# Kernel optimization log

Hardware: AMD Instinct MI355X
Metric: run time of the kernel (lower is better)

Reference implementation:

```python
import jax, jax.numpy as jnp
import numpy as np

D = 1024
H = 16
DK = D // H
MLP = 4096
EPS = 1e-5


def layernorm(x, w, b):
    mu = jnp.mean(x, axis=-1, keepdims=True)
    var = jnp.mean(jnp.square(x - mu), axis=-1, keepdims=True)
    return (x - mu) * jax.lax.rsqrt(var + EPS) * w + b


def setup_inputs() -> dict:
    key = jax.random.key(0)
    ks = jax.random.split(key, 12)
    s = 0.02
    return {
        "x": jax.random.normal(ks[0], (8, 1024, D), dtype=jnp.float32),
        "ln1_w": jnp.ones((D,), jnp.float32),
        "ln1_b": jnp.zeros((D,), jnp.float32),
        "wq": jax.random.normal(ks[1], (D, D), jnp.float32) * s,
        "bq": jnp.zeros((D,), jnp.float32),
        "wk": jax.random.normal(ks[2], (D, D), jnp.float32) * s,
        "bk": jnp.zeros((D,), jnp.float32),
        "wv": jax.random.normal(ks[3], (D, D), jnp.float32) * s,
        "bv": jnp.zeros((D,), jnp.float32),
        "wo": jax.random.normal(ks[4], (D, D), jnp.float32) * s,
        "bo": jnp.zeros((D,), jnp.float32),
        "ln2_w": jnp.ones((D,), jnp.float32),
        "ln2_b": jnp.zeros((D,), jnp.float32),
        "w1": jax.random.normal(ks[5], (D, MLP), jnp.float32) * s,
        "b1": jnp.zeros((MLP,), jnp.float32),
        "w2": jax.random.normal(ks[6], (MLP, D), jnp.float32) * s,
        "b2": jnp.zeros((D,), jnp.float32),
    }


def reference(x, ln1_w, ln1_b, wq, bq, wk, bk, wv, bv, wo, bo, ln2_w, ln2_b, w1, b1, w2, b2):
    B, S, _ = x.shape
    h = layernorm(x, ln1_w, ln1_b)
    # QKV projections, split heads: [B, H, S, DK]
    q = (h @ wq + bq).reshape(B, S, H, DK).transpose(0, 2, 1, 3)
    k = (h @ wk + bk).reshape(B, S, H, DK).transpose(0, 2, 1, 3)
    v = (h @ wv + bv).reshape(B, S, H, DK).transpose(0, 2, 1, 3)
    scores = jnp.einsum('bhqd,bhkd->bhqk', q, k) / np.sqrt(DK).astype(np.float32)
    attn = jax.nn.softmax(scores, axis=-1)
    ctx = jnp.einsum('bhqk,bhkd->bhqd', attn, v)
    ctx = ctx.transpose(0, 2, 1, 3).reshape(B, S, D)
    # NOTE: original MultiHeadAttention applies ReLU after the output projection
    attn_out = jax.nn.relu(ctx @ wo + bo)
    out1 = x + attn_out  # dropout is identity in eval
    h2 = layernorm(out1, ln2_w, ln2_b)
    ff = jax.nn.gelu(h2 @ w1 + b1, approximate=False) @ w2 + b2
    return out1 + ff
```

## Files before the change

### kernel.cpp

```cpp
#include <hip/hip_runtime.h>
#include <hip/hip_bf16.h>
#include <math.h>

typedef __bf16 bf16x8 __attribute__((ext_vector_type(8)));
typedef __bf16 bf16x4 __attribute__((ext_vector_type(4)));
typedef float f32x4 __attribute__((ext_vector_type(4)));

typedef __attribute__((address_space(3))) unsigned int lds_u32_t;
typedef __attribute__((address_space(1))) const unsigned int glb_u32_t;

static __device__ __forceinline__ f32x4 mfma16(bf16x8 a, bf16x8 b, f32x4 c) {
  return __builtin_amdgcn_mfma_f32_16x16x32_bf16(a, b, c, 0, 0, 0);
}

static __device__ __forceinline__ float fast_exp2(float x) {
#if __has_builtin(__builtin_amdgcn_exp2f)
  return __builtin_amdgcn_exp2f(x);
#else
  return exp2f(x);
#endif
}

static __device__ __forceinline__ void load_lds16(const __bf16* g, __bf16* l) {
  __builtin_amdgcn_global_load_lds((glb_u32_t*)g, (lds_u32_t*)l, 16, 0, 0);
}

__global__ __launch_bounds__(256) void transpose_w(const float* __restrict__ src,
                                                   __bf16* __restrict__ dst,
                                                   int R, int C) {
  __shared__ float tile[32][33];
  int tx = threadIdx.x, ty = threadIdx.y;
  int c0 = blockIdx.x * 32, r0 = blockIdx.y * 32;
#pragma unroll
  for (int i = 0; i < 4; i++)
    tile[ty + 8 * i][tx] = src[(size_t)(r0 + ty + 8 * i) * C + c0 + tx];
  __syncthreads();
#pragma unroll
  for (int i = 0; i < 4; i++)
    dst[(size_t)(c0 + ty + 8 * i) * R + r0 + tx] = (__bf16)tile[tx][ty + 8 * i];
}

__global__ __launch_bounds__(256) void ln_kernel(const float* __restrict__ x,
                                                 const float* __restrict__ w,
                                                 const float* __restrict__ b,
                                                 __bf16* __restrict__ out) {
  int row = blockIdx.x, tid = threadIdx.x;
  const float* xr = x + (size_t)row * 1024;
  float v[4];
  float s = 0.f, sq = 0.f;
#pragma unroll
  for (int i = 0; i < 4; i++) {
    v[i] = xr[tid + 256 * i];
    s += v[i];
    sq += v[i] * v[i];
  }
#pragma unroll
  for (int off = 1; off < 64; off <<= 1) {
    s += __shfl_xor(s, off, 64);
    sq += __shfl_xor(sq, off, 64);
  }
  __shared__ float red[8];
  int wave = tid >> 6, lane = tid & 63;
  if (lane == 0) { red[wave] = s; red[4 + wave] = sq; }
  __syncthreads();
  if (tid == 0) {
    float S = red[0] + red[1] + red[2] + red[3];
    float SQ = red[4] + red[5] + red[6] + red[7];
    float mu = S * (1.f / 1024.f);
    float var = SQ * (1.f / 1024.f) - mu * mu;
    red[0] = mu;
    red[1] = rsqrtf(var + 1e-5f);
  }
  __syncthreads();
  float mu = red[0], rstd = red[1];
  __bf16* orow = out + (size_t)row * 1024;
#pragma unroll
  for (int i = 0; i < 4; i++) {
    int c = tid + 256 * i;
    orow[c] = (__bf16)((v[i] - mu) * rstd * w[c] + b[c]);
  }
}

enum { MODE_QKV = 0, MODE_WO = 3, MODE_F1 = 4, MODE_F2 = 5 };

template <int MODE>
__global__ __launch_bounds__(256, 2) void gemm_bt(const __bf16* __restrict__ A,
                                                  const __bf16* __restrict__ Bt,
                                                  const float* __restrict__ b0,
                                                  const float* __restrict__ b1,
                                                  const float* __restrict__ b2,
                                                  const float* __restrict__ aux,
                                                  void* __restrict__ o0,
                                                  void* __restrict__ o1,
                                                  void* __restrict__ o2,
                                                  int N, int K) {
  __shared__ __align__(16) __bf16 As[128 * 64];
  __shared__ __align__(16) __bf16 Bs[128 * 64];
  const int tid = threadIdx.x;
  const int m0 = blockIdx.y * 128, n0 = blockIdx.x * 128;
  const int wave = tid >> 6, lane = tid & 63, quad = lane >> 4, l16 = lane & 15;
  const int wm = (wave >> 1) * 64, wn = (wave & 1) * 64;

  int srow[4], sgran[4];
#pragma unroll
  for (int i = 0; i < 4; i++) {
    int inst = wave * 4 + i;
    srow[i] = inst * 8 + (lane >> 3);
    sgran[i] = (lane & 7) ^ (srow[i] & 7);
  }

  const f32x4 zero4 = {0.f, 0.f, 0.f, 0.f};
  f32x4 acc[4][4];
#pragma unroll
  for (int i = 0; i < 4; i++)
#pragma unroll
    for (int j = 0; j < 4; j++) acc[i][j] = zero4;

  for (int kt = 0; kt < K; kt += 64) {
#pragma unroll
    for (int i = 0; i < 4; i++) {
      int inst = wave * 4 + i;
      load_lds16(&A[(size_t)(m0 + srow[i]) * K + kt + sgran[i] * 8], &As[inst * 512]);
      load_lds16(&Bt[(size_t)(n0 + srow[i]) * K + kt + sgran[i] * 8], &Bs[inst * 512]);
    }
    __syncthreads();
#pragma unroll
    for (int ks = 0; ks < 64; ks += 32) {
      bf16x8 af[4], bfv[4];
#pragma unroll
      for (int mi = 0; mi < 4; mi++) {
        int row = wm + 16 * mi + l16;
        int pg = ((ks >> 3) + quad) ^ (row & 7);
        af[mi] = *(const bf16x8*)&As[row * 64 + pg * 8];
      }
#pragma unroll
      for (int ni = 0; ni < 4; ni++) {
        int row = wn + 16 * ni + l16;
        int pg = ((ks >> 3) + quad) ^ (row & 7);
        bfv[ni] = *(const bf16x8*)&Bs[row * 64 + pg * 8];
      }
#pragma unroll
      for (int mi = 0; mi < 4; mi++)
#pragma unroll
        for (int ni = 0; ni < 4; ni++)
          acc[mi][ni] = mfma16(af[mi], bfv[ni], acc[mi][ni]);
    }
    __syncthreads();
  }

  int seg = (n0 >> 10);
  const float* bsel = (MODE == MODE_QKV) ? (seg == 0 ? b0 : seg == 1 ? b1 : b2) : b0;

#pragma unroll
  for (int mi = 0; mi < 4; mi++) {
#pragma unroll
    for (int ni = 0; ni < 4; ni++) {
      int ncol = n0 + wn + 16 * ni + l16;
      int cc = ncol & 1023;
      float bval = bsel[(MODE == MODE_QKV) ? cc : ncol];
#pragma unroll
      for (int r = 0; r < 4; r++) {
        int m = m0 + wm + 16 * mi + quad * 4 + r;
        float val = acc[mi][ni][r] + bval;
        if constexpr (MODE == MODE_QKV) {
          int bb = m >> 10, s = m & 1023, h = cc >> 6, dk = cc & 63;
          if (seg == 0)
            ((__bf16*)o0)[(((size_t)(bb * 16 + h)) * 1024 + s) * 64 + dk] =
                (__bf16)(val * 0.18033688011112042f);
          else if (seg == 1)
            ((__bf16*)o1)[(((size_t)(bb * 16 + h)) * 1024 + s) * 64 + dk] = (__bf16)val;
          else
            ((__bf16*)o2)[(((size_t)(bb * 16 + h)) * 64 + dk) * 1024 + s] = (__bf16)val;
        } else if constexpr (MODE == MODE_WO) {
          val = fmaxf(val, 0.f);
          size_t idx = (size_t)m * 1024 + ncol;
          ((float*)o0)[idx] = aux[idx] + val;
        } else if constexpr (MODE == MODE_F1) {
          float g = 0.5f * val * (1.f + erff(val * 0.70710678118654752f));
          ((__bf16*)o0)[(size_t)m * 4096 + ncol] = (__bf16)g;
        } else {
          size_t idx = (size_t)m * 1024 + ncol;
          ((float*)o0)[idx] = aux[idx] + val;
        }
      }
    }
  }
}

template <int MODE>
__global__ __launch_bounds__(512, 2) void gemm256(const __bf16* __restrict__ A,
                                                  const __bf16* __restrict__ Bt,
                                                  const float* __restrict__ b0,
                                                  const float* __restrict__ b1,
                                                  const float* __restrict__ b2,
                                                  const float* __restrict__ aux,
                                                  void* __restrict__ o0,
                                                  void* __restrict__ o1,
                                                  void* __restrict__ o2,
                                                  int N, int K) {
  __shared__ __align__(16) __bf16 As[4][8192];
  __shared__ __align__(16) __bf16 Bs[4][8192];
  const int tid = threadIdx.x;
  const int m0 = blockIdx.y * 256, n0 = blockIdx.x * 256;
  const int wave = tid >> 6, lane = tid & 63, quad = lane >> 4, l16 = lane & 15;
  const int wr = wave >> 2, wc = wave & 3;

  const int Lsub = lane >> 3;
  const int sp = (lane & 7) ^ Lsub;
  const int par = sp & 1, kq = sp >> 1;
  const int rbase = wave * 16 + 2 * Lsub + par;
  const __bf16* pA0 = A + (size_t)(m0 + rbase) * K + 8 * kq;
  const __bf16* pA1 = A + (size_t)(m0 + rbase + 128) * K + 8 * kq;
  const __bf16* pB0 = Bt + (size_t)(n0 + rbase) * K + 8 * kq;
  const __bf16* pB1 = Bt + (size_t)(n0 + rbase + 128) * K + 8 * kq;
  const int dst0 = (wave * 8) * 64;
  const int dst1 = (64 + wave * 8) * 64;

  int afOff[8], bfOff[4];
#pragma unroll
  for (int mi = 0; mi < 8; mi++) {
    int r = wr * 128 + 16 * mi + l16;
    int L = r >> 1;
    int sl = (2 * quad + (r & 1)) ^ (L & 7);
    afOff[mi] = L * 128 + sl * 16;
  }
#pragma unroll
  for (int nj = 0; nj < 4; nj++) {
    int c = wc * 64 + 16 * nj + l16;
    int L = c >> 1;
    int sl = (2 * quad + (c & 1)) ^ (L & 7);
    bfOff[nj] = L * 128 + sl * 16;
  }

  const f32x4 zero4 = {0.f, 0.f, 0.f, 0.f};
  f32x4 acc[8][4];
#pragma unroll
  for (int i = 0; i < 8; i++)
#pragma unroll
    for (int j = 0; j < 4; j++) acc[i][j] = zero4;

  const int nt = K >> 5;

  auto stage = [&](int t) {
    int slot = t & 3;
    __bf16* a = &As[slot][0];
    __bf16* b = &Bs[slot][0];
    load_lds16(pA0, a + dst0);
    load_lds16(pA1, a + dst1);
    load_lds16(pB0, b + dst0);
    load_lds16(pB1, b + dst1);
    pA0 += 32; pA1 += 32; pB0 += 32; pB1 += 32;
  };

  auto window = [&](int t, bool dostage) {
    const char* ab = (const char*)&As[t & 3][0];
    const char* bb = (const char*)&Bs[t & 3][0];
    bf16x8 af[8], bfv[4];
#pragma unroll
    for (int mi = 0; mi < 8; mi++) af[mi] = *(const bf16x8*)(ab + afOff[mi]);
#pragma unroll
    for (int nj = 0; nj < 4; nj++) bfv[nj] = *(const bf16x8*)(bb + bfOff[nj]);
    if (dostage) stage(t + 3);
    __builtin_amdgcn_s_setprio(1);
#pragma unroll
    for (int mi = 0; mi < 8; mi++)
#pragma unroll
      for (int nj = 0; nj < 4; nj++)
        acc[mi][nj] = mfma16(af[mi], bfv[nj], acc[mi][nj]);
    __builtin_amdgcn_s_setprio(0);
  };

  stage(0);
  stage(1);
  stage(2);
  asm volatile("s_waitcnt vmcnt(8)" ::: "memory");
  __builtin_amdgcn_s_barrier();
  __builtin_amdgcn_sched_barrier(0);

  for (int t = 0; t < nt - 3; ++t) {
    window(t, true);
    asm volatile("s_waitcnt vmcnt(8)" ::: "memory");
    __builtin_amdgcn_s_barrier();
    __builtin_amdgcn_sched_barrier(0);
  }
  window(nt - 3, false);
  asm volatile("s_waitcnt vmcnt(4)" ::: "memory");
  __builtin_amdgcn_s_barrier();
  __builtin_amdgcn_sched_barrier(0);
  window(nt - 2, false);
  asm volatile("s_waitcnt vmcnt(0)" ::: "memory");
  __builtin_amdgcn_s_barrier();
  __builtin_amdgcn_sched_barrier(0);
  window(nt - 1, false);

  int seg = (n0 >> 10);
  const float* bsel = (MODE == MODE_QKV) ? (seg == 0 ? b0 : seg == 1 ? b1 : b2) : b0;

#pragma unroll
  for (int mi = 0; mi < 8; mi++) {
#pragma unroll
    for (int nj = 0; nj < 4; nj++) {
      int ncol = n0 + wc * 64 + 16 * nj + l16;
      int cc = ncol & 1023;
      float bval = bsel[(MODE == MODE_QKV) ? cc : ncol];
#pragma unroll
      for (int r = 0; r < 4; r++) {
        int m = m0 + wr * 128 + 16 * mi + quad * 4 + r;
        float val = acc[mi][nj][r] + bval;
        if constexpr (MODE == MODE_QKV) {
          int bb = m >> 10, s = m & 1023, h = cc >> 6, dk = cc & 63;
          if (seg == 0)
            ((__bf16*)o0)[(((size_t)(bb * 16 + h)) * 1024 + s) * 64 + dk] =
                (__bf16)(val * 0.18033688011112042f);
          else if (seg == 1)
            ((__bf16*)o1)[(((size_t)(bb * 16 + h)) * 1024 + s) * 64 + dk] = (__bf16)val;
          else
            ((__bf16*)o2)[(((size_t)(bb * 16 + h)) * 64 + dk) * 1024 + s] = (__bf16)val;
        } else if constexpr (MODE == MODE_WO) {
          val = fmaxf(val, 0.f);
          size_t idx = (size_t)m * 1024 + ncol;
          ((float*)o0)[idx] = aux[idx] + val;
        } else if constexpr (MODE == MODE_F1) {
          float g = 0.5f * val * (1.f + erff(val * 0.70710678118654752f));
          ((__bf16*)o0)[(size_t)m * 4096 + ncol] = (__bf16)g;
        } else {
          size_t idx = (size_t)m * 1024 + ncol;
          ((float*)o0)[idx] = aux[idx] + val;
        }
      }
    }
  }
}

__global__ __launch_bounds__(256) void attn_kernel(const __bf16* __restrict__ Q,
                                                   const __bf16* __restrict__ Kp,
                                                   const __bf16* __restrict__ Vt,
                                                   __bf16* __restrict__ ctx) {
  __shared__ __align__(16) __bf16 Ps[2][4][32][72];
  const int tid = threadIdx.x;
  const int bh = blockIdx.x, qb = blockIdx.y;
  const int wave = tid >> 6, lane = tid & 63, quad = lane >> 4, l16 = lane & 15;
  const int qrow0 = qb * 128 + wave * 32;

  bf16x8 aq[2][2];
#pragma unroll
  for (int mi = 0; mi < 2; mi++) {
    const __bf16* qrow = Q + ((size_t)bh * 1024 + qrow0 + mi * 16 + l16) * 64;
    aq[mi][0] = *(const bf16x8*)&qrow[8 * quad];
    aq[mi][1] = *(const bf16x8*)&qrow[32 + 8 * quad];
  }

  const f32x4 zero4 = {0.f, 0.f, 0.f, 0.f};
  f32x4 o[2][4];
  float lp[2] = {0.f, 0.f};
#pragma unroll
  for (int mi = 0; mi < 2; mi++)
#pragma unroll
    for (int nj = 0; nj < 4; nj++) o[mi][nj] = zero4;

  const __bf16* kb0 = Kp + (size_t)bh * 65536;
  const __bf16* vb0 = Vt + (size_t)bh * 65536;

  bf16x8 kfA[4][2], kfB[4][2];
#pragma unroll
  for (int ni = 0; ni < 4; ni++) {
    const __bf16* krow = kb0 + (16 * ni + l16) * 64;
    kfA[ni][0] = *(const bf16x8*)&krow[8 * quad];
    kfA[ni][1] = *(const bf16x8*)&krow[32 + 8 * quad];
  }

  auto body = [&](int kbk, int buf, bf16x8 (&kcur)[4][2], bf16x8 (&knxt)[4][2]) {
    bf16x8 vf[2][4];
#pragma unroll
    for (int half = 0; half < 2; half++)
#pragma unroll
      for (int nj = 0; nj < 4; nj++)
        vf[half][nj] = *(const bf16x8*)(vb0 + (size_t)(nj * 16 + l16) * 1024 +
                                        kbk * 64 + 32 * half + 8 * quad);
    if (kbk < 15) {
      const __bf16* kbase = kb0 + (kbk + 1) * 4096;
#pragma unroll
      for (int ni = 0; ni < 4; ni++) {
        const __bf16* krow = kbase + (16 * ni + l16) * 64;
        knxt[ni][0] = *(const bf16x8*)&krow[8 * quad];
        knxt[ni][1] = *(const bf16x8*)&krow[32 + 8 * quad];
      }
    }
    f32x4 st[2][4];
    __builtin_amdgcn_s_setprio(1);
#pragma unroll
    for (int mi = 0; mi < 2; mi++)
#pragma unroll
      for (int ni = 0; ni < 4; ni++) {
        st[mi][ni] = mfma16(kcur[ni][0], aq[mi][0], zero4);
        st[mi][ni] = mfma16(kcur[ni][1], aq[mi][1], st[mi][ni]);
      }
    __builtin_amdgcn_s_setprio(0);
#pragma unroll
    for (int mi = 0; mi < 2; mi++)
#pragma unroll
      for (int ni = 0; ni < 4; ni++) {
        union { bf16x4 v4; __bf16 b[4]; } pk;
#pragma unroll
        for (int r = 0; r < 4; r++) {
          float p = fast_exp2(st[mi][ni][r]);
          lp[mi] += p;
          pk.b[r] = (__bf16)p;
        }
        *(bf16x4*)&Ps[buf][wave][16 * mi + l16][16 * ni + 4 * quad] = pk.v4;
      }
    bf16x8 pa[2][2];
#pragma unroll
    for (int mi = 0; mi < 2; mi++) {
      pa[mi][0] = *(const bf16x8*)&Ps[buf][wave][16 * mi + l16][8 * quad];
      pa[mi][1] = *(const bf16x8*)&Ps[buf][wave][16 * mi + l16][32 + 8 * quad];
    }
    __builtin_amdgcn_s_setprio(1);
#pragma unroll
    for (int mi = 0; mi < 2; mi++)
#pragma unroll
      for (int nj = 0; nj < 4; nj++) {
        o[mi][nj] = mfma16(pa[mi][0], vf[0][nj], o[mi][nj]);
        o[mi][nj] = mfma16(pa[mi][1], vf[1][nj], o[mi][nj]);
      }
    __builtin_amdgcn_s_setprio(0);
  };

  for (int kbk2 = 0; kbk2 < 16; kbk2 += 2) {
    body(kbk2, 0, kfA, kfB);
    body(kbk2 + 1, 1, kfB, kfA);
  }

#pragma unroll
  for (int mi = 0; mi < 2; mi++) {
    lp[mi] += __shfl_xor(lp[mi], 16, 64);
    lp[mi] += __shfl_xor(lp[mi], 32, 64);
  }

  int bb = bh >> 4, h = bh & 15;
#pragma unroll
  for (int mi = 0; mi < 2; mi++)
#pragma unroll
    for (int r = 0; r < 4; r++) {
      float inv = 1.f / __shfl(lp[mi], 4 * quad + r, 64);
      int s = qrow0 + mi * 16 + 4 * quad + r;
#pragma unroll
      for (int nj = 0; nj < 4; nj++)
        ctx[((size_t)(bb * 1024 + s)) * 1024 + h * 64 + nj * 16 + l16] =
            (__bf16)(o[mi][nj][r] * inv);
    }
}

extern "C" void kernel_launch(void* const* d_in, const int* in_sizes, int n_in,
                              void* d_out, int out_size, void* d_ws, size_t ws_size,
                              hipStream_t stream) {
  const float* x = (const float*)d_in[0];
  const float* ln1w = (const float*)d_in[1];
  const float* ln1b = (const float*)d_in[2];
  const float* wq = (const float*)d_in[3];
  const float* bq = (const float*)d_in[4];
  const float* wk = (const float*)d_in[5];
  const float* bk = (const float*)d_in[6];
  const float* wv = (const float*)d_in[7];
  const float* bv = (const float*)d_in[8];
  const float* wo = (const float*)d_in[9];
  const float* bo = (const float*)d_in[10];
  const float* ln2w = (const float*)d_in[11];
  const float* ln2b = (const float*)d_in[12];
  const float* w1 = (const float*)d_in[13];
  const float* b1 = (const float*)d_in[14];
  const float* w2 = (const float*)d_in[15];
  const float* b2 = (const float*)d_in[16];
  float* out = (float*)d_out;

  char* ws = (char*)d_ws;
  const size_t MB = 1024 * 1024;
  __bf16* wqkv_t = (__bf16*)(ws + 0 * MB);
  __bf16* wq_t = (__bf16*)(ws + 0 * MB);
  __bf16* wk_t = (__bf16*)(ws + 2 * MB);
  __bf16* wv_t = (__bf16*)(ws + 4 * MB);
  __bf16* wo_t = (__bf16*)(ws + 6 * MB);
  __bf16* w1_t = (__bf16*)(ws + 8 * MB);
  __bf16* w2_t = (__bf16*)(ws + 16 * MB);
  __bf16* hbuf = (__bf16*)(ws + 24 * MB);
  __bf16* qbuf = (__bf16*)(ws + 40 * MB);
  __bf16* kbuf = (__bf16*)(ws + 56 * MB);
  __bf16* vtbuf = (__bf16*)(ws + 72 * MB);
  __bf16* ctxbuf = (__bf16*)(ws + 88 * MB);
  __bf16* ff1 = (__bf16*)(ws + 40 * MB);

  dim3 tb(32, 8);
  transpose_w<<<dim3(32, 32), tb, 0, stream>>>(wq, wq_t, 1024, 1024);
  transpose_w<<<dim3(32, 32), tb, 0, stream>>>(wk, wk_t, 1024, 1024);
  transpose_w<<<dim3(32, 32), tb, 0, stream>>>(wv, wv_t, 1024, 1024);
  transpose_w<<<dim3(32, 32), tb, 0, stream>>>(wo, wo_t, 1024, 1024);
  transpose_w<<<dim3(128, 32), tb, 0, stream>>>(w1, w1_t, 1024, 4096);
  transpose_w<<<dim3(32, 128), tb, 0, stream>>>(w2, w2_t, 4096, 1024);

  ln_kernel<<<8192, 256, 0, stream>>>(x, ln1w, ln1b, hbuf);

  gemm256<MODE_QKV><<<dim3(12, 32), 512, 0, stream>>>(
      hbuf, wqkv_t, bq, bk, bv, nullptr, qbuf, kbuf, vtbuf, 3072, 1024);

  attn_kernel<<<dim3(128, 8), 256, 0, stream>>>(qbuf, kbuf, vtbuf, ctxbuf);

  gemm_bt<MODE_WO><<<dim3(8, 64), 256, 0, stream>>>(
      ctxbuf, wo_t, bo, nullptr, nullptr, x, out, nullptr, nullptr, 1024, 1024);

  ln_kernel<<<8192, 256, 0, stream>>>(out, ln2w, ln2b, hbuf);

  gemm256<MODE_F1><<<dim3(16, 32), 512, 0, stream>>>(
      hbuf, w1_t, b1, nullptr, nullptr, nullptr, ff1, nullptr, nullptr, 4096, 1024);
  gemm_bt<MODE_F2><<<dim3(8, 64), 256, 0, stream>>>(
      ff1, w2_t, b2, nullptr, nullptr, out, out, nullptr, nullptr, 1024, 4096);
}
```

Baseline: 595.2 us.

## Halve attention query tile per wave and double grid for occupancy

The attention kernel now handles 16 query rows per wave instead of 32, doubles the grid along the query axis, and adds a launch-bounds occupancy hint of 4 blocks. K and V fragments are prefetched one key block ahead inside a simple loop rather than a ping-pong lambda. The aim is to cut register pressure and raise occupancy to hide global-load latency. The cost is that each K/V fragment is reused by half as many query rows, so K/V global traffic doubles.

```diff
diff --git a/kernel.cpp b/kernel.cpp
--- a/kernel.cpp
+++ b/kernel.cpp
@@ -332,123 +332,108 @@
   }
 }
 
-__global__ __launch_bounds__(256) void attn_kernel(const __bf16* __restrict__ Q,
-                                                   const __bf16* __restrict__ Kp,
-                                                   const __bf16* __restrict__ Vt,
-                                                   __bf16* __restrict__ ctx) {
-  __shared__ __align__(16) __bf16 Ps[2][4][32][72];
+__global__ __launch_bounds__(256, 4) void attn_kernel(const __bf16* __restrict__ Q,
+                                                      const __bf16* __restrict__ Kp,
+                                                      const __bf16* __restrict__ Vt,
+                                                      __bf16* __restrict__ ctx) {
+  __shared__ __align__(16) __bf16 Ps[2][4][16][72];
   const int tid = threadIdx.x;
   const int bh = blockIdx.x, qb = blockIdx.y;
   const int wave = tid >> 6, lane = tid & 63, quad = lane >> 4, l16 = lane & 15;
-  const int qrow0 = qb * 128 + wave * 32;
-
-  bf16x8 aq[2][2];
-#pragma unroll
-  for (int mi = 0; mi < 2; mi++) {
-    const __bf16* qrow = Q + ((size_t)bh * 1024 + qrow0 + mi * 16 + l16) * 64;
-    aq[mi][0] = *(const bf16x8*)&qrow[8 * quad];
-    aq[mi][1] = *(const bf16x8*)&qrow[32 + 8 * quad];
+  const int qrow0 = qb * 64 + wave * 16;
+
+  bf16x8 aq[2];
+  {
+    const __bf16* qrow = Q + ((size_t)bh * 1024 + qrow0 + l16) * 64;
+    aq[0] = *(const bf16x8*)&qrow[8 * quad];
+    aq[1] = *(const bf16x8*)&qrow[32 + 8 * quad];
   }
 
   const f32x4 zero4 = {0.f, 0.f, 0.f, 0.f};
-  f32x4 o[2][4];
-  float lp[2] = {0.f, 0.f};
-#pragma unroll
-  for (int mi = 0; mi < 2; mi++)
-#pragma unroll
-    for (int nj = 0; nj < 4; nj++) o[mi][nj] = zero4;
+  f32x4 o[4];
+  float lp = 0.f;
+#pragma unroll
+  for (int nj = 0; nj < 4; nj++) o[nj] = zero4;
 
   const __bf16* kb0 = Kp + (size_t)bh * 65536;
   const __bf16* vb0 = Vt + (size_t)bh * 65536;
 
-  bf16x8 kfA[4][2], kfB[4][2];
+  bf16x8 kf[4][2], vf[2][4];
 #pragma unroll
   for (int ni = 0; ni < 4; ni++) {
     const __bf16* krow = kb0 + (16 * ni + l16) * 64;
-    kfA[ni][0] = *(const bf16x8*)&krow[8 * quad];
-    kfA[ni][1] = *(const bf16x8*)&krow[32 + 8 * quad];
-  }
-
-  auto body = [&](int kbk, int buf, bf16x8 (&kcur)[4][2], bf16x8 (&knxt)[4][2]) {
-    bf16x8 vf[2][4];
-#pragma unroll
-    for (int half = 0; half < 2; half++)
-#pragma unroll
-      for (int nj = 0; nj < 4; nj++)
-        vf[half][nj] = *(const bf16x8*)(vb0 + (size_t)(nj * 16 + l16) * 1024 +
-                                        kbk * 64 + 32 * half + 8 * quad);
-    if (kbk < 15) {
-      const __bf16* kbase = kb0 + (kbk + 1) * 4096;
+    kf[ni][0] = *(const bf16x8*)&krow[8 * quad];
+    kf[ni][1] = *(const bf16x8*)&krow[32 + 8 * quad];
+  }
+#pragma unroll
+  for (int half = 0; half < 2; half++)
+#pragma unroll
+    for (int nj = 0; nj < 4; nj++)
+      vf[half][nj] = *(const bf16x8*)(vb0 + (size_t)(nj * 16 + l16) * 1024 +
+                                      32 * half + 8 * quad);
+
+  for (int t = 0; t < 16; ++t) {
+    const int buf = t & 1;
+    f32x4 st[4];
+    __builtin_amdgcn_s_setprio(1);
+#pragma unroll
+    for (int ni = 0; ni < 4; ni++) {
+      st[ni] = mfma16(kf[ni][0], aq[0], zero4);
+      st[ni] = mfma16(kf[ni][1], aq[1], st[ni]);
+    }
+    __builtin_amdgcn_s_setprio(0);
+    if (t < 15) {
+      const __bf16* kbase = kb0 + (t + 1) * 4096;
 #pragma unroll
       for (int ni = 0; ni < 4; ni++) {
         const __bf16* krow = kbase + (16 * ni + l16) * 64;
-        knxt[ni][0] = *(const bf16x8*)&krow[8 * quad];
-        knxt[ni][1] = *(const bf16x8*)&krow[32 + 8 * quad];
+        kf[ni][0] = *(const bf16x8*)&krow[8 * quad];
+        kf[ni][1] = *(const bf16x8*)&krow[32 + 8 * quad];
       }
     }
-    f32x4 st[2][4];
+#pragma unroll
+    for (int ni = 0; ni < 4; ni++) {
+      union { bf16x4 v4; __bf16 b[4]; } pk;
+#pragma unroll
+      for (int r = 0; r < 4; r++) {
+        float p = fast_exp2(st[ni][r]);
+        lp += p;
+        pk.b[r] = (__bf16)p;
+      }
+      *(bf16x4*)&Ps[buf][wave][l16][16 * ni + 4 * quad] = pk.v4;
+    }
+    bf16x8 pa0 = *(const bf16x8*)&Ps[buf][wave][l16][8 * quad];
+    bf16x8 pa1 = *(const bf16x8*)&Ps[buf][wave][l16][32 + 8 * quad];
     __builtin_amdgcn_s_setprio(1);
 #pragma unroll
-    for (int mi = 0; mi < 2; mi++)
-#pragma unroll
-      for (int ni = 0; ni < 4; ni++) {
-        st[mi][ni] = mfma16(kcur[ni][0], aq[mi][0], zero4);
-        st[mi][ni] = mfma16(kcur[ni][1], aq[mi][1], st[mi][ni]);
-      }
+    for (int nj = 0; nj < 4; nj++) {
+      o[nj] = mfma16(pa0, vf[0][nj], o[nj]);
+      o[nj] = mfma16(pa1, vf[1][nj], o[nj]);
+    }
     __builtin_amdgcn_s_setprio(0);
-#pragma unroll
-    for (int mi = 0; mi < 2; mi++)
-#pragma unroll
-      for (int ni = 0; ni < 4; ni++) {
-        union { bf16x4 v4; __bf16 b[4]; } pk;
-#pragma unroll
-        for (int r = 0; r < 4; r++) {
-          float p = fast_exp2(st[mi][ni][r]);
-          lp[mi] += p;
-          pk.b[r] = (__bf16)p;
-        }
-        *(bf16x4*)&Ps[buf][wave][16 * mi + l16][16 * ni + 4 * quad] = pk.v4;
-      }
-    bf16x8 pa[2][2];
-#pragma unroll
-    for (int mi = 0; mi < 2; mi++) {
-      pa[mi][0] = *(const bf16x8*)&Ps[buf][wave][16 * mi + l16][8 * quad];
-      pa[mi][1] = *(const bf16x8*)&Ps[buf][wave][16 * mi + l16][32 + 8 * quad];
-    }
-    __builtin_amdgcn_s_setprio(1);
-#pragma unroll
-    for (int mi = 0; mi < 2; mi++)
-#pragma unroll
-      for (int nj = 0; nj < 4; nj++) {
-        o[mi][nj] = mfma16(pa[mi][0], vf[0][nj], o[mi][nj]);
-        o[mi][nj] = mfma16(pa[mi][1], vf[1][nj], o[mi][nj]);
-      }
-    __builtin_amdgcn_s_setprio(0);
-  };
-
-  for (int kbk2 = 0; kbk2 < 16; kbk2 += 2) {
-    body(kbk2, 0, kfA, kfB);
-    body(kbk2 + 1, 1, kfB, kfA);
-  }
-
-#pragma unroll
-  for (int mi = 0; mi < 2; mi++) {
-    lp[mi] += __shfl_xor(lp[mi], 16, 64);
-    lp[mi] += __shfl_xor(lp[mi], 32, 64);
-  }
+    if (t < 15) {
+#pragma unroll
+      for (int half = 0; half < 2; half++)
+#pragma unroll
+        for (int nj = 0; nj < 4; nj++)
+          vf[half][nj] = *(const bf16x8*)(vb0 + (size_t)(nj * 16 + l16) * 1024 +
+                                          (t + 1) * 64 + 32 * half + 8 * quad);
+    }
+  }
+
+  lp += __shfl_xor(lp, 16, 64);
+  lp += __shfl_xor(lp, 32, 64);
 
   int bb = bh >> 4, h = bh & 15;
 #pragma unroll
-  for (int mi = 0; mi < 2; mi++)
-#pragma unroll
-    for (int r = 0; r < 4; r++) {
-      float inv = 1.f / __shfl(lp[mi], 4 * quad + r, 64);
-      int s = qrow0 + mi * 16 + 4 * quad + r;
-#pragma unroll
-      for (int nj = 0; nj < 4; nj++)
-        ctx[((size_t)(bb * 1024 + s)) * 1024 + h * 64 + nj * 16 + l16] =
-            (__bf16)(o[mi][nj][r] * inv);
-    }
+  for (int r = 0; r < 4; r++) {
+    float inv = 1.f / __shfl(lp, 4 * quad + r, 64);
+    int s = qrow0 + 4 * quad + r;
+#pragma unroll
+    for (int nj = 0; nj < 4; nj++)
+      ctx[((size_t)(bb * 1024 + s)) * 1024 + h * 64 + nj * 16 + l16] =
+          (__bf16)(o[nj][r] * inv);
+  }
 }
 
 extern "C" void kernel_launch(void* const* d_in, const int* in_sizes, int n_in,
@@ -502,7 +487,7 @@
   gemm256<MODE_QKV><<<dim3(12, 32), 512, 0, stream>>>(
       hbuf, wqkv_t, bq, bk, bv, nullptr, qbuf, kbuf, vtbuf, 3072, 1024);
 
-  attn_kernel<<<dim3(128, 8), 256, 0, stream>>>(qbuf, kbuf, vtbuf, ctxbuf);
+  attn_kernel<<<dim3(128, 16), 256, 0, stream>>>(qbuf, kbuf, vtbuf, ctxbuf);
 
   gemm_bt<MODE_WO><<<dim3(8, 64), 256, 0, stream>>>(
       ctxbuf, wo_t, bo, nullptr, nullptr, x, out, nullptr, nullptr, 1024, 1024);
```

Result: slower. 696.6 us (+17.0%).

## Stage K and V tiles through swizzled LDS with double-buffered async loads

Applied to the files above, without the earlier changes.

The attention kernel now stages each 64-key K and V tile into shared memory, double-buffered, using async global-to-LDS loads with an XOR swizzle. It replaces the old per-wave direct global loads, where every wave fetched the same K/V fragments on its own. Waves now share one staged copy and read fragments from LDS, which cuts redundant global traffic. In exchange it adds a block barrier per tile and a vmcnt(0) wait, and the launch bound now asks for 2 blocks per CU, which may constrain registers.

```diff
diff --git a/kernel.cpp b/kernel.cpp
--- a/kernel.cpp
+++ b/kernel.cpp
@@ -332,10 +332,12 @@
   }
 }
 
-__global__ __launch_bounds__(256) void attn_kernel(const __bf16* __restrict__ Q,
-                                                   const __bf16* __restrict__ Kp,
-                                                   const __bf16* __restrict__ Vt,
-                                                   __bf16* __restrict__ ctx) {
+__global__ __launch_bounds__(256, 2) void attn_kernel(const __bf16* __restrict__ Q,
+                                                      const __bf16* __restrict__ Kp,
+                                                      const __bf16* __restrict__ Vt,
+                                                      __bf16* __restrict__ ctx) {
+  __shared__ __align__(16) __bf16 Ks[2][64][64];
+  __shared__ __align__(16) __bf16 Vs[2][64][64];
   __shared__ __align__(16) __bf16 Ps[2][4][32][72];
   const int tid = threadIdx.x;
   const int bh = blockIdx.x, qb = blockIdx.y;
@@ -361,30 +363,46 @@
   const __bf16* kb0 = Kp + (size_t)bh * 65536;
   const __bf16* vb0 = Vt + (size_t)bh * 65536;
 
-  bf16x8 kfA[4][2], kfB[4][2];
+  const int srow = lane >> 3;
+  const int sgran = (lane & 7) ^ srow;
+  const int r0 = wave * 16;
+
+  auto stage = [&](int t) {
+    int buf = t & 1;
+    const __bf16* ks = kb0 + (size_t)(t * 64 + r0 + srow) * 64 + sgran * 8;
+    load_lds16(ks, &Ks[buf][r0][0]);
+    load_lds16(ks + 8 * 64, &Ks[buf][r0 + 8][0]);
+    const __bf16* vs = vb0 + (size_t)(r0 + srow) * 1024 + t * 64 + sgran * 8;
+    load_lds16(vs, &Vs[buf][r0][0]);
+    load_lds16(vs + 8 * 1024, &Vs[buf][r0 + 8][0]);
+  };
+
+  int kOff[4][2], vOff[4][2];
 #pragma unroll
   for (int ni = 0; ni < 4; ni++) {
-    const __bf16* krow = kb0 + (16 * ni + l16) * 64;
-    kfA[ni][0] = *(const bf16x8*)&krow[8 * quad];
-    kfA[ni][1] = *(const bf16x8*)&krow[32 + 8 * quad];
-  }
-
-  auto body = [&](int kbk, int buf, bf16x8 (&kcur)[4][2], bf16x8 (&knxt)[4][2]) {
-    bf16x8 vf[2][4];
-#pragma unroll
-    for (int half = 0; half < 2; half++)
-#pragma unroll
-      for (int nj = 0; nj < 4; nj++)
-        vf[half][nj] = *(const bf16x8*)(vb0 + (size_t)(nj * 16 + l16) * 1024 +
-                                        kbk * 64 + 32 * half + 8 * quad);
-    if (kbk < 15) {
-      const __bf16* kbase = kb0 + (kbk + 1) * 4096;
-#pragma unroll
-      for (int ni = 0; ni < 4; ni++) {
-        const __bf16* krow = kbase + (16 * ni + l16) * 64;
-        knxt[ni][0] = *(const bf16x8*)&krow[8 * quad];
-        knxt[ni][1] = *(const bf16x8*)&krow[32 + 8 * quad];
-      }
+    int r = 16 * ni + l16;
+#pragma unroll
+    for (int half = 0; half < 2; half++) {
+      int g = quad + 4 * half;
+      kOff[ni][half] = r * 128 + ((g ^ (r & 7)) * 16);
+      vOff[ni][half] = kOff[ni][half];
+    }
+  }
+
+  stage(0);
+  asm volatile("s_waitcnt vmcnt(0)" ::: "memory");
+  __builtin_amdgcn_s_barrier();
+
+  for (int t = 0; t < 16; ++t) {
+    const int buf = t & 1;
+    if (t < 15) stage(t + 1);
+    const char* kbuf_ = (const char*)&Ks[buf][0][0];
+    const char* vbuf_ = (const char*)&Vs[buf][0][0];
+    bf16x8 kf[4][2];
+#pragma unroll
+    for (int ni = 0; ni < 4; ni++) {
+      kf[ni][0] = *(const bf16x8*)(kbuf_ + kOff[ni][0]);
+      kf[ni][1] = *(const bf16x8*)(kbuf_ + kOff[ni][1]);
     }
     f32x4 st[2][4];
     __builtin_amdgcn_s_setprio(1);
@@ -392,10 +410,16 @@
     for (int mi = 0; mi < 2; mi++)
 #pragma unroll
       for (int ni = 0; ni < 4; ni++) {
-        st[mi][ni] = mfma16(kcur[ni][0], aq[mi][0], zero4);
-        st[mi][ni] = mfma16(kcur[ni][1], aq[mi][1], st[mi][ni]);
+        st[mi][ni] = mfma16(kf[ni][0], aq[mi][0], zero4);
+        st[mi][ni] = mfma16(kf[ni][1], aq[mi][1], st[mi][ni]);
       }
     __builtin_amdgcn_s_setprio(0);
+    bf16x8 vf[2][4];
+#pragma unroll
+    for (int nj = 0; nj < 4; nj++) {
+      vf[0][nj] = *(const bf16x8*)(vbuf_ + vOff[nj][0]);
+      vf[1][nj] = *(const bf16x8*)(vbuf_ + vOff[nj][1]);
+    }
 #pragma unroll
     for (int mi = 0; mi < 2; mi++)
 #pragma unroll
@@ -424,11 +448,10 @@
         o[mi][nj] = mfma16(pa[mi][1], vf[1][nj], o[mi][nj]);
       }
     __builtin_amdgcn_s_setprio(0);
-  };
-
-  for (int kbk2 = 0; kbk2 < 16; kbk2 += 2) {
-    body(kbk2, 0, kfA, kfB);
-    body(kbk2 + 1, 1, kfB, kfA);
+    if (t < 15) {
+      asm volatile("s_waitcnt vmcnt(0)" ::: "memory");
+      __builtin_amdgcn_s_barrier();
+    }
   }
 
 #pragma unroll
```

New measurement: 528.8 us. 11.2% less time.
